# Performance work log

Measured on AMD Instinct MI355X. Metric: run time of the kernel, lower is better.

Reference implementation:

```python
import jax, jax.numpy as jnp
import numpy as np

B, D, L = 8192, 2048, 4


def setup_inputs() -> dict:
    key = jax.random.key(0)
    kx, kw = jax.random.split(key)
    x = jax.random.normal(kx, (B, D), dtype=jnp.float32)
    # truncated_normal(stddev=0.01) approximated by scaled normal
    W = jax.random.normal(kw, (L, D), dtype=jnp.float32) * 0.01
    b = jnp.zeros((L, D), dtype=jnp.float32)
    return {"x": x, "W": W, "b": b}


def reference(x, W, b):
    # DCN cross layers. The original materializes the (B, d, d) outer product
    # o[b,j,k] = cross[b,j] * x0[b,k], multiplies by W[i] (broadcast over k)
    # and sums over j with keepdims. That reduces exactly to
    #   (sum_j cross[b,j]) * x0[b,k] * W[i,k]
    # so we compute the fused O(B*d) form (same math, no d^2 intermediate).
    x0 = x
    cross = x
    for i in range(W.shape[0]):
        s = jnp.sum(cross, axis=1, keepdims=True)        # (B, 1)
        cross = s * x0 * W[i] + b[i] + cross             # (B, d)
    return cross  # Flatten of (B, d) is identity
```

## Files before the change

### kernel.cpp

```cpp
#include <hip/hip_runtime.h>


typedef float v4 __attribute__((ext_vector_type(4)));

constexpr int Bn = 8192;
constexpr int D = 2048;
constexpr int L = 4;
constexpr int THREADS = 256;
constexpr int VEC = 4;
constexpr int PASSES = D / (THREADS * VEC);
constexpr int RPB = 8;
constexpr int GRID = Bn / RPB;

__device__ inline float hsum(v4 v) { return v.x + v.y + v.z + v.w; }

template <int CTRL>
__device__ inline float dpp_add(float x) {
    int xi = __builtin_bit_cast(int, x);
    int yi = __builtin_amdgcn_update_dpp(0, xi, CTRL, 0xf, 0xf, true);
    return x + __builtin_bit_cast(float, yi);
}
__device__ inline float wave_sum(float x) {
    x = dpp_add<0x111>(x);
    x = dpp_add<0x112>(x);
    x = dpp_add<0x114>(x);
    x = dpp_add<0x118>(x);
    x = dpp_add<0x142>(x);
    x = dpp_add<0x143>(x);
    return x;
}

__global__ __launch_bounds__(THREADS) void cross_layer_kernel(
    const float* __restrict__ x,
    const float* __restrict__ W,
    const float* __restrict__ b,
    float* __restrict__ out)
{
    const int tid = threadIdx.x;
    const int lane = tid & 63;
    const int wid = tid >> 6;
    const int col = tid * VEC;

    __shared__ float redp[4][3];
    __shared__ float red[2][4][4];

    v4 xv[PASSES], xn[PASSES];
    {
        const float* xr = x + (size_t)blockIdx.x * D;
#pragma unroll
        for (int p = 0; p < PASSES; ++p)
            xv[p] = *reinterpret_cast<const v4*>(xr + p * (THREADS * VEC) + col);
    }

    v4 wv[L][PASSES];
    v4 bs[PASSES];
    float bred[3] = {0.f, 0.f, 0.f};

#pragma unroll
    for (int p = 0; p < PASSES; ++p) {
        const int d = p * (THREADS * VEC) + col;
        v4 bsum = {0.f, 0.f, 0.f, 0.f};
#pragma unroll
        for (int i = 0; i < L; ++i) {
            wv[i][p] = *reinterpret_cast<const v4*>(W + i * D + d);
            v4 bb = *reinterpret_cast<const v4*>(b + i * D + d);
            bsum += bb;
            if (i < 3) bred[i] += hsum(bb);
        }
        bs[p] = bsum;
    }

#pragma unroll
    for (int k = 0; k < 3; ++k) bred[k] = wave_sum(bred[k]);
    if (lane == 63)
#pragma unroll
        for (int k = 0; k < 3; ++k) redp[wid][k] = bred[k];
    __syncthreads();
    float Bsc[3];
#pragma unroll
    for (int k = 0; k < 3; ++k)
        Bsc[k] = redp[0][k] + redp[1][k] + redp[2][k] + redp[3][k];

#pragma unroll
    for (int k = 0; k < RPB; ++k) {
        if (k + 1 < RPB) {
            const float* xr = x + (size_t)(blockIdx.x + GRID * (k + 1)) * D;
#pragma unroll
            for (int p = 0; p < PASSES; ++p)
                xn[p] = *reinterpret_cast<const v4*>(xr + p * (THREADS * VEC) + col);
        }

        float sm[4] = {0.f, 0.f, 0.f, 0.f};
#pragma unroll
        for (int p = 0; p < PASSES; ++p) {
            sm[0] += hsum(xv[p]);
#pragma unroll
            for (int i = 0; i < 3; ++i)
                sm[1 + i] += hsum(xv[p] * wv[i][p]);
        }
#pragma unroll
        for (int q = 0; q < 4; ++q) sm[q] = wave_sum(sm[q]);

        if (lane == 63)
#pragma unroll
            for (int q = 0; q < 4; ++q) red[k & 1][wid][q] = sm[q];
        __syncthreads();

        const float T = red[k & 1][0][0] + red[k & 1][1][0]
                      + red[k & 1][2][0] + red[k & 1][3][0];
        float A[3];
#pragma unroll
        for (int q = 0; q < 3; ++q)
            A[q] = red[k & 1][0][1 + q] + red[k & 1][1][1 + q]
                 + red[k & 1][2][1 + q] + red[k & 1][3][1 + q];

        float s[L];
        s[0] = T;
#pragma unroll
        for (int i = 1; i < L; ++i)
            s[i] = s[i - 1] * (1.f + A[i - 1]) + Bsc[i - 1];

        float* outr = out + (size_t)(blockIdx.x + GRID * k) * D;
#pragma unroll
        for (int p = 0; p < PASSES; ++p) {
            v4 c = {1.f, 1.f, 1.f, 1.f};
#pragma unroll
            for (int i = 0; i < L; ++i)
                c += s[i] * wv[i][p];
            *reinterpret_cast<v4*>(outr + p * (THREADS * VEC) + col)
                = xv[p] * c + bs[p];
        }

#pragma unroll
        for (int p = 0; p < PASSES; ++p) xv[p] = xn[p];
    }
}

extern "C" void kernel_launch(void* const* d_in, const int* in_sizes, int n_in,
                              void* d_out, int out_size, void* d_ws, size_t ws_size,
                              hipStream_t stream) {
    const float* x = (const float*)d_in[0];
    const float* W = (const float*)d_in[1];
    const float* b = (const float*)d_in[2];
    float* out = (float*)d_out;
    cross_layer_kernel<<<GRID, THREADS, 0, stream>>>(x, W, b, out);
}
```

Measured before the change: 26.41 us.

## Split fused cross kernel into scalar-reduction pass and streaming output pass

Splits the single fused kernel into two launches when enough workspace is available. The first computes the per-row scalar coefficients (row sums and dot products with W) into a small table, and the second re-reads x and streams the output using those scalars with no block-level reduction or barrier. The aim is to take the reduction and __syncthreads off the critical path of the store-heavy pass. In exchange x is read twice from memory and there is an extra kernel launch.

```diff
diff --git a/kernel.cpp b/kernel.cpp
--- a/kernel.cpp
+++ b/kernel.cpp
@@ -30,7 +30,159 @@
     return x;
 }
 
-__global__ __launch_bounds__(THREADS) void cross_layer_kernel(
+__global__ __launch_bounds__(THREADS) void scalars_kernel(
+    const float* __restrict__ x,
+    const float* __restrict__ W,
+    const float* __restrict__ b,
+    float* __restrict__ stab)
+{
+    const int tid = threadIdx.x;
+    const int lane = tid & 63;
+    const int wid = tid >> 6;
+    const int col = tid * VEC;
+
+    __shared__ float redp[4][3];
+    __shared__ float red[2][4][4];
+
+    v4 xv[PASSES], xn[PASSES];
+    {
+        const float* xr = x + (size_t)blockIdx.x * D;
+#pragma unroll
+        for (int p = 0; p < PASSES; ++p)
+            xv[p] = *reinterpret_cast<const v4*>(xr + p * (THREADS * VEC) + col);
+    }
+
+    v4 wv[3][PASSES];
+    float bred[3] = {0.f, 0.f, 0.f};
+#pragma unroll
+    for (int p = 0; p < PASSES; ++p) {
+        const int d = p * (THREADS * VEC) + col;
+#pragma unroll
+        for (int i = 0; i < 3; ++i) {
+            wv[i][p] = *reinterpret_cast<const v4*>(W + i * D + d);
+            bred[i] += hsum(*reinterpret_cast<const v4*>(b + i * D + d));
+        }
+    }
+#pragma unroll
+    for (int k = 0; k < 3; ++k) bred[k] = wave_sum(bred[k]);
+    if (lane == 63)
+#pragma unroll
+        for (int k = 0; k < 3; ++k) redp[wid][k] = bred[k];
+    __syncthreads();
+    float Bsc[3];
+#pragma unroll
+    for (int k = 0; k < 3; ++k)
+        Bsc[k] = redp[0][k] + redp[1][k] + redp[2][k] + redp[3][k];
+
+#pragma unroll
+    for (int k = 0; k < RPB; ++k) {
+        if (k + 1 < RPB) {
+            const float* xr = x + (size_t)(blockIdx.x + GRID * (k + 1)) * D;
+#pragma unroll
+            for (int p = 0; p < PASSES; ++p)
+                xn[p] = *reinterpret_cast<const v4*>(xr + p * (THREADS * VEC) + col);
+        }
+
+        float sm[4] = {0.f, 0.f, 0.f, 0.f};
+#pragma unroll
+        for (int p = 0; p < PASSES; ++p) {
+            sm[0] += hsum(xv[p]);
+#pragma unroll
+            for (int i = 0; i < 3; ++i)
+                sm[1 + i] += hsum(xv[p] * wv[i][p]);
+        }
+#pragma unroll
+        for (int q = 0; q < 4; ++q) sm[q] = wave_sum(sm[q]);
+
+        if (lane == 63)
+#pragma unroll
+            for (int q = 0; q < 4; ++q) red[k & 1][wid][q] = sm[q];
+        __syncthreads();
+
+        if (tid == 0) {
+            const float T = red[k & 1][0][0] + red[k & 1][1][0]
+                          + red[k & 1][2][0] + red[k & 1][3][0];
+            float A[3];
+#pragma unroll
+            for (int q = 0; q < 3; ++q)
+                A[q] = red[k & 1][0][1 + q] + red[k & 1][1][1 + q]
+                     + red[k & 1][2][1 + q] + red[k & 1][3][1 + q];
+            v4 s;
+            s.x = T;
+            s.y = s.x * (1.f + A[0]) + Bsc[0];
+            s.z = s.y * (1.f + A[1]) + Bsc[1];
+            s.w = s.z * (1.f + A[2]) + Bsc[2];
+            *reinterpret_cast<v4*>(stab + ((size_t)blockIdx.x + GRID * k) * 4) = s;
+        }
+
+#pragma unroll
+        for (int p = 0; p < PASSES; ++p) xv[p] = xn[p];
+    }
+}
+
+__global__ __launch_bounds__(THREADS) void stream_kernel(
+    const float* __restrict__ x,
+    const float* __restrict__ W,
+    const float* __restrict__ b,
+    const float* __restrict__ stab,
+    float* __restrict__ out)
+{
+    const int tid = threadIdx.x;
+    const int col = tid * VEC;
+
+    v4 xv[PASSES], xn[PASSES];
+    {
+        const float* xr = x + (size_t)blockIdx.x * D;
+#pragma unroll
+        for (int p = 0; p < PASSES; ++p)
+            xv[p] = *reinterpret_cast<const v4*>(xr + p * (THREADS * VEC) + col);
+    }
+    v4 sv = *reinterpret_cast<const v4*>(stab + (size_t)blockIdx.x * 4);
+
+    v4 wv[L][PASSES];
+    v4 bs[PASSES];
+#pragma unroll
+    for (int p = 0; p < PASSES; ++p) {
+        const int d = p * (THREADS * VEC) + col;
+        v4 bsum = {0.f, 0.f, 0.f, 0.f};
+#pragma unroll
+        for (int i = 0; i < L; ++i) {
+            wv[i][p] = *reinterpret_cast<const v4*>(W + i * D + d);
+            bsum += *reinterpret_cast<const v4*>(b + i * D + d);
+        }
+        bs[p] = bsum;
+    }
+
+#pragma unroll
+    for (int k = 0; k < RPB; ++k) {
+        v4 sn;
+        if (k + 1 < RPB) {
+            const float* xr = x + (size_t)(blockIdx.x + GRID * (k + 1)) * D;
+#pragma unroll
+            for (int p = 0; p < PASSES; ++p)
+                xn[p] = *reinterpret_cast<const v4*>(xr + p * (THREADS * VEC) + col);
+            sn = *reinterpret_cast<const v4*>(stab + ((size_t)blockIdx.x + GRID * (k + 1)) * 4);
+        }
+
+        float* outr = out + ((size_t)blockIdx.x + GRID * k) * D;
+#pragma unroll
+        for (int p = 0; p < PASSES; ++p) {
+            v4 c = {1.f, 1.f, 1.f, 1.f};
+            c += sv.x * wv[0][p];
+            c += sv.y * wv[1][p];
+            c += sv.z * wv[2][p];
+            c += sv.w * wv[3][p];
+            *reinterpret_cast<v4*>(outr + p * (THREADS * VEC) + col)
+                = xv[p] * c + bs[p];
+        }
+
+#pragma unroll
+        for (int p = 0; p < PASSES; ++p) xv[p] = xn[p];
+        sv = sn;
+    }
+}
+
+__global__ __launch_bounds__(THREADS) void cross_layer_fused(
     const float* __restrict__ x,
     const float* __restrict__ W,
     const float* __restrict__ b,
@@ -55,7 +207,6 @@
     v4 wv[L][PASSES];
     v4 bs[PASSES];
     float bred[3] = {0.f, 0.f, 0.f};
-
 #pragma unroll
     for (int p = 0; p < PASSES; ++p) {
         const int d = p * (THREADS * VEC) + col;
@@ -69,7 +220,6 @@
         }
         bs[p] = bsum;
     }
-
 #pragma unroll
     for (int k = 0; k < 3; ++k) bred[k] = wave_sum(bred[k]);
     if (lane == 63)
@@ -120,7 +270,7 @@
         for (int i = 1; i < L; ++i)
             s[i] = s[i - 1] * (1.f + A[i - 1]) + Bsc[i - 1];
 
-        float* outr = out + (size_t)(blockIdx.x + GRID * k) * D;
+        float* outr = out + ((size_t)blockIdx.x + GRID * k) * D;
 #pragma unroll
         for (int p = 0; p < PASSES; ++p) {
             v4 c = {1.f, 1.f, 1.f, 1.f};
@@ -143,5 +293,13 @@
     const float* W = (const float*)d_in[1];
     const float* b = (const float*)d_in[2];
     float* out = (float*)d_out;
-    cross_layer_kernel<<<GRID, THREADS, 0, stream>>>(x, W, b, out);
-}
+
+    const size_t table_bytes = (size_t)Bn * 4 * sizeof(float);
+    if (ws_size >= table_bytes) {
+        float* stab = (float*)d_ws;
+        scalars_kernel<<<GRID, THREADS, 0, stream>>>(x, W, b, stab);
+        stream_kernel<<<GRID, THREADS, 0, stream>>>(x, W, b, stab, out);
+    } else {
+        cross_layer_fused<<<GRID, THREADS, 0, stream>>>(x, W, b, out);
+    }
+}
```

Result: slower. 38.92 us (+47.4%).
